# Kernel tuning notes

Measured on AMD Instinct MI355X. Metric: run time of the kernel, lower is better.

Reference implementation:

```python
import jax, jax.numpy as jnp
import numpy as np

B = 256
# (Cin, Cout, K, Hout) for each of the 6 deformable conv layers; input is 33x33
_LAYERS = [(1, 16, 3, 31), (16, 32, 3, 29), (32, 16, 5, 25), (16, 16, 7, 19), (16, 8, 5, 15), (8, 4, 3, 13)]


def setup_inputs() -> dict:
    key = jax.random.key(0)
    ks = jax.random.split(key, 24)
    inp = {"x": jax.random.normal(ks[0], (B, 1, 33, 33), dtype=jnp.float32)}
    for i, (ci, co, k, ho) in enumerate(_LAYERS):
        inp[f"off{i+1}"] = jax.random.normal(ks[1 + i], (1, 2 * k * k, ho, ho), dtype=jnp.float32)
        inp[f"w{i+1}"] = jax.random.normal(ks[7 + i], (co, ci, k, k), dtype=jnp.float32) / float(np.sqrt(ci * k * k))
        inp[f"b{i+1}"] = jnp.zeros((co,), jnp.float32)
    inp["w7"] = jax.random.normal(ks[13], (13 * 13 * 4, 256), dtype=jnp.float32) / 26.0
    inp["b7"] = jnp.zeros((256,), jnp.float32)
    inp["w8"] = jax.random.normal(ks[14], (256, 10), dtype=jnp.float32) / 16.0
    inp["b8"] = jnp.zeros((10,), jnp.float32)
    inp["perm"] = jnp.arange(13 * 13, dtype=jnp.int32)  # fixed spatial permutation (perm_6.ordenar)
    return inp


def _deform_conv(x, offset, weight, bias):
    # torchvision DeformConv2d, stride=1, padding=0, fixed offsets shared across batch.
    Bn, Cin, H, W = x.shape
    Cout, _, K, _ = weight.shape
    Ho, Wo = offset.shape[-2], offset.shape[-1]
    K2 = K * K
    off = offset[0].reshape(K2, 2, Ho, Wo)  # channel layout: [2k]=dy, [2k+1]=dx
    ky, kx = jnp.meshgrid(jnp.arange(K), jnp.arange(K), indexing='ij')
    py = jnp.arange(Ho, dtype=x.dtype)[None, :, None] + ky.reshape(-1, 1, 1) + off[:, 0]  # [K2,Ho,Wo]
    px = jnp.arange(Wo, dtype=x.dtype)[None, None, :] + kx.reshape(-1, 1, 1) + off[:, 1]
    y0f = jnp.floor(py); x0f = jnp.floor(px)
    wy = py - y0f; wx = px - x0f
    y0 = y0f.astype(jnp.int32); x0 = x0f.astype(jnp.int32)
    xf = x.reshape(Bn, Cin, H * W)

    def gather(yi, xi):
        valid = ((yi >= 0) & (yi < H) & (xi >= 0) & (xi < W)).astype(x.dtype)
        idx = (jnp.clip(yi, 0, H - 1) * W + jnp.clip(xi, 0, W - 1)).reshape(-1)
        v = xf[:, :, idx].reshape(Bn, Cin, K2, Ho, Wo)
        return v * valid[None, None]

    s = (gather(y0, x0) * ((1 - wy) * (1 - wx))[None, None]
         + gather(y0, x0 + 1) * ((1 - wy) * wx)[None, None]
         + gather(y0 + 1, x0) * (wy * (1 - wx))[None, None]
         + gather(y0 + 1, x0 + 1) * (wy * wx)[None, None])  # [B,Cin,K2,Ho,Wo]
    out = jnp.einsum('bckhw,ock->bohw', s, weight.reshape(Cout, Cin, K2))
    return out + bias[None, :, None, None]


def reference(x, off1, off2, off3, off4, off5, off6,
              w1, b1, w2, b2, w3, b3, w4, b4, w5, b5, w6, b6,
              w7, b7, w8, b8, perm):
    offs = (off1, off2, off3, off4, off5, off6)
    ws = (w1, w2, w3, w4, w5, w6)
    bs = (b1, b2, b3, b4, b5, b6)
    for off, w, b in zip(offs, ws, bs):
        x = jax.nn.relu(_deform_conv(x, off, w, b))
    Bn = x.shape[0]
    x = x.reshape(Bn, 4, 13 * 13)[:, :, perm].reshape(Bn, -1)  # perm_6.ordenar as spatial permutation
    h = jax.nn.relu(x @ w7 + b7)
    return h @ w8 + b8
```

## Files before the change

kernel.cpp:

```cpp
#include <hip/hip_runtime.h>

template<int N> struct IC { static constexpr int val = N; };

struct WtArgs { const float* src[6]; int co[6], ci[6], k2[6], dstoff[6]; };

__global__ __launch_bounds__(256)
void transpose_weights(WtArgs a, float* __restrict__ dst0)
{
    const int L = blockIdx.x;
    const float* __restrict__ s = a.src[L];
    float* __restrict__ d = dst0 + a.dstoff[L];
    const int co = a.co[L], ci = a.ci[L], k2 = a.k2[L];
    const int n = co * ci * k2;
    for (int i = threadIdx.x; i < n; i += 256) {
        int k = i % k2;
        int c = (i / k2) % ci;
        int o = i / (k2 * ci);
        d[(k * ci + c) * co + o] = s[i];
    }
}

struct MetaArgs { const float* off[6]; int P[6], K[6], WO[6], H[6], W[6], base[6]; };

__global__ __launch_bounds__(256)
void build_meta(MetaArgs a, float* __restrict__ meta0)
{
    const int L = blockIdx.y;
    const float* __restrict__ off = a.off[L];
    const int P = a.P[L], K = a.K[L], WOv = a.WO[L], H = a.H[L], Wv = a.W[L];
    const int N = P * K * K;
    float* __restrict__ m = meta0 + (size_t)a.base[L] * 8;
    for (int e = blockIdx.x * 256 + threadIdx.x; e < N; e += gridDim.x * 256) {
        const int k = e / P, p = e - k * P;
        const int ho = p / WOv, wo = p - ho * WOv;
        const int ky = k / K, kx = k - ky * K;
        const float dy = off[(2 * k)     * P + p];
        const float dx = off[(2 * k + 1) * P + p];
        const float py = (float)(ho + ky) + dy;
        const float px = (float)(wo + kx) + dx;
        const float y0f = floorf(py), x0f = floorf(px);
        const float wy = py - y0f, wx = px - x0f;
        const int y0 = (int)y0f, x0 = (int)x0f;
        const int y1 = y0 + 1,  x1 = x0 + 1;
        const bool vy0 = ((unsigned)y0 < (unsigned)H);
        const bool vy1 = ((unsigned)y1 < (unsigned)H);
        const bool vx0 = ((unsigned)x0 < (unsigned)Wv);
        const bool vx1 = ((unsigned)x1 < (unsigned)Wv);
        const int cy0 = min(max(y0, 0), H - 1) * Wv;
        const int cy1 = min(max(y1, 0), H - 1) * Wv;
        const int cx0 = min(max(x0, 0), Wv - 1);
        const int cx1 = min(max(x1, 0), Wv - 1);
        int4 mi;
        mi.x = cy0 + cx0; mi.y = cy0 + cx1; mi.z = cy1 + cx0; mi.w = cy1 + cx1;
        float4 mw;
        mw.x = (vy0 && vx0) ? (1.f - wy) * (1.f - wx) : 0.f;
        mw.y = (vy0 && vx1) ? (1.f - wy) * wx         : 0.f;
        mw.z = (vy1 && vx0) ? wy * (1.f - wx)         : 0.f;
        mw.w = (vy1 && vx1) ? wy * wx                 : 0.f;
        *(int4*)(m + (size_t)e * 8)       = mi;
        *(float4*)(m + (size_t)e * 8 + 4) = mw;
    }
}

template<int CIN, int CINW, int COUT, int K, int H, int W, int HO, int WO,
         int S, int KSEG, int NT, int NCOMB, bool SPLITOUT, bool MET,
         int NSL = 1, int CINL = 0, int NCHS = 1, int KSPL = 1>
__global__ __launch_bounds__(NT)
void deform_lds(const float* __restrict__ x0, const float* __restrict__ x1,
                const float* __restrict__ x2, const float* __restrict__ x3,
                const float* __restrict__ off, const float* __restrict__ meta,
                const float* __restrict__ wT, const float* __restrict__ bias,
                float* __restrict__ y, size_t pstride)
{
    constexpr int K2 = K * K, HW = H * W, P = HO * WO;
    constexpr int PW = ((P + 63) / 64) * 64;
    constexpr int K2B  = (K2 + KSPL - 1) / KSPL;
    constexpr int KLEN = (K2B + KSEG - 1) / KSEG;
    constexpr int PSTR = (COUT % 2 == 0) ? COUT + 1 : COUT;
    static_assert(NT >= KSEG * PW, "NT too small for KSEG*PW");

    __shared__ __align__(16) float simg[HW * S];
    __shared__ float part[(KSEG > 1) ? (KSEG - 1) * P * PSTR : 1];

    const int tid = threadIdx.x;
    const int b   = blockIdx.x;
    const int hy  = SPLITOUT ? blockIdx.y : 0;
    const int hch = (KSPL > 1) ? (hy % NCHS) : hy;
    const int hk  = (KSPL > 1) ? (hy / NCHS) : 0;

    const size_t xoff = (size_t)b * CINW * HW + (SPLITOUT ? (size_t)hch * CIN * HW : 0);
    const float* xb  = x0 + xoff;
    const float* xb1 = (NCOMB >= 2) ? (x1 + xoff) : nullptr;
    const float* xb2 = (NCOMB >= 3) ? (x2 + xoff) : nullptr;
    const float* xb3 = (NCOMB >= 4) ? (x3 + xoff) : nullptr;
    for (int i = tid; i < CIN * HW; i += NT) {
        int c = i / HW, hw = i - c * HW;
        bool ok = true;
        if constexpr (SPLITOUT) ok = (hch * CIN + c < CINW);
        float v = 0.f;
        if (ok) {
            v = xb[i];
            if constexpr (NCOMB >= 2) v += xb1[i];
            if constexpr (NCOMB >= 3) v += xb2[i];
            if constexpr (NCOMB >= 4) v += xb3[i];
            if constexpr (NCOMB >= 2) v = fmaxf(v, 0.f);
        }
        simg[hw * S + c] = v;
    }
    __syncthreads();

    const int g  = tid / PW;
    const int p  = tid - g * PW;
    const int pc = (p < P) ? p : (P - 1);
    const bool active = (p < P);

    float acc[COUT];
#pragma unroll
    for (int o = 0; o < COUT; ++o) acc[o] = 0.f;

    if (g < KSEG) {
        if ((!SPLITOUT || hy == 0) && g == 0) {
#pragma unroll
            for (int o = 0; o < COUT; ++o) acc[o] = bias[o];
        }
        const int ho = pc / WO, wo = pc - ho * WO;
        const int kb   = hk * K2B + g * KLEN;
        const int kend = (KSPL > 1) ? min(K2, hk * K2B + K2B) : K2;

        auto run = [&](auto nc4tag) {
            constexpr int NC4 = decltype(nc4tag)::val;

            auto fma_block = [&](int i00, int i01, int i10, int i11,
                                 float w00, float w01, float w10, float w11,
                                 int kku) {
                const float* __restrict__ r00 = simg + i00 * S;
                const float* __restrict__ r01 = simg + i01 * S;
                const float* __restrict__ r10 = simg + i10 * S;
                const float* __restrict__ r11 = simg + i11 * S;
                const float* __restrict__ wk = wT + kku * (CINW * COUT)
                                             + (SPLITOUT ? hch * (CIN * COUT) : 0);
                if constexpr (CIN % 4 == 0) {
#pragma unroll
                    for (int c4 = 0; c4 < NC4; ++c4) {
                        const float4 v00 = *(const float4*)(r00 + c4 * 4);
                        const float4 v01 = *(const float4*)(r01 + c4 * 4);
                        const float4 v10 = *(const float4*)(r10 + c4 * 4);
                        const float4 v11 = *(const float4*)(r11 + c4 * 4);
                        float4 sa;
                        sa.x = fmaf(w00, v00.x, fmaf(w01, v01.x, fmaf(w10, v10.x, w11 * v11.x)));
                        sa.y = fmaf(w00, v00.y, fmaf(w01, v01.y, fmaf(w10, v10.y, w11 * v11.y)));
                        sa.z = fmaf(w00, v00.z, fmaf(w01, v01.z, fmaf(w10, v10.z, w11 * v11.z)));
                        sa.w = fmaf(w00, v00.w, fmaf(w01, v01.w, fmaf(w10, v10.w, w11 * v11.w)));
                        const float* __restrict__ wc = wk + (c4 * 4) * COUT;
#pragma unroll
                        for (int o = 0; o < COUT; ++o) acc[o] = fmaf(wc[o], sa.x, acc[o]);
#pragma unroll
                        for (int o = 0; o < COUT; ++o) acc[o] = fmaf(wc[COUT + o], sa.y, acc[o]);
#pragma unroll
                        for (int o = 0; o < COUT; ++o) acc[o] = fmaf(wc[2 * COUT + o], sa.z, acc[o]);
#pragma unroll
                        for (int o = 0; o < COUT; ++o) acc[o] = fmaf(wc[3 * COUT + o], sa.w, acc[o]);
                    }
                } else {
#pragma unroll
                    for (int c = 0; c < CIN; ++c) {
                        float sa = fmaf(w00, r00[c], fmaf(w01, r01[c],
                                   fmaf(w10, r10[c], w11 * r11[c])));
#pragma unroll
                        for (int o = 0; o < COUT; ++o)
                            acc[o] = fmaf(wk[c * COUT + o], sa, acc[o]);
                    }
                }
            };

            if constexpr (MET) {
                const int kf = (kb < K2) ? kb : (K2 - 1);
                int4   nmi = *(const int4*)  (meta + (size_t)(kf * P + pc) * 8);
                float4 nmw = *(const float4*)(meta + (size_t)(kf * P + pc) * 8 + 4);

#pragma unroll 1
                for (int j = 0; j < KLEN; ++j) {
                    const int k  = kb + j;
                    const int kk = (k < K2) ? k : (K2 - 1);
                    const int4   mi  = nmi;
                    const float4 mwv = nmw;
                    const int kn = (k + 1 < K2) ? (k + 1) : (K2 - 1);
                    nmi = *(const int4*)  (meta + (size_t)(kn * P + pc) * 8);
                    nmw = *(const float4*)(meta + (size_t)(kn * P + pc) * 8 + 4);

                    float w00 = mwv.x, w01 = mwv.y, w10 = mwv.z, w11 = mwv.w;
                    if constexpr (K2 % (KSEG * KSPL) != 0) {
                        const float kv = (k < kend) ? 1.f : 0.f;
                        w00 *= kv; w01 *= kv; w10 *= kv; w11 *= kv;
                    }
                    const int kku = __builtin_amdgcn_readfirstlane(kk);
                    fma_block(mi.x, mi.y, mi.z, mi.w, w00, w01, w10, w11, kku);
                }
            } else {
                const int kf = (kb < K2) ? kb : (K2 - 1);
                float ndy = off[(2 * kf)     * P + pc];
                float ndx = off[(2 * kf + 1) * P + pc];

#pragma unroll 1
                for (int j = 0; j < KLEN; ++j) {
                    const int k  = kb + j;
                    const int kk = (k < K2) ? k : (K2 - 1);
                    const float dy = ndy, dx = ndx;
                    const int kn = (k + 1 < K2) ? (k + 1) : (K2 - 1);
                    ndy = off[(2 * kn)     * P + pc];
                    ndx = off[(2 * kn + 1) * P + pc];

                    const int ky = kk / K, kx = kk - ky * K;
                    const float py = (float)(ho + ky) + dy;
                    const float px = (float)(wo + kx) + dx;
                    const float y0f = floorf(py), x0f = floorf(px);
                    const float wy = py - y0f, wx = px - x0f;
                    const int y0 = (int)y0f, x0 = (int)x0f;
                    const int y1 = y0 + 1,  x1i = x0 + 1;
                    const bool vy0 = ((unsigned)y0  < (unsigned)H);
                    const bool vy1 = ((unsigned)y1  < (unsigned)H);
                    const bool vx0 = ((unsigned)x0  < (unsigned)W);
                    const bool vx1 = ((unsigned)x1i < (unsigned)W);
                    const int cy0 = min(max(y0, 0), H - 1) * W;
                    const int cy1 = min(max(y1, 0), H - 1) * W;
                    const int cx0 = min(max(x0, 0), W - 1);
                    const int cx1 = min(max(x1i, 0), W - 1);
                    float w00 = (vy0 && vx0) ? (1.f - wy) * (1.f - wx) : 0.f;
                    float w01 = (vy0 && vx1) ? (1.f - wy) * wx         : 0.f;
                    float w10 = (vy1 && vx0) ? wy * (1.f - wx)         : 0.f;
                    float w11 = (vy1 && vx1) ? wy * wx                 : 0.f;
                    if constexpr (K2 % (KSEG * KSPL) != 0) {
                        const float kv = (k < kend) ? 1.f : 0.f;
                        w00 *= kv; w01 *= kv; w10 *= kv; w11 *= kv;
                    }
                    const int kku = __builtin_amdgcn_readfirstlane(kk);
                    fma_block(cy0 + cx0, cy0 + cx1, cy1 + cx0, cy1 + cx1,
                              w00, w01, w10, w11, kku);
                }
            }
        };

        if constexpr (SPLITOUT && CINL > 0) {
            if (hch == NSL - 1) run(IC<(CINL + 3) / 4>{});
            else                run(IC<(CIN + 3) / 4>{});
        } else {
            run(IC<(CIN + 3) / 4>{});
        }

        if (g > 0 && active) {
#pragma unroll
            for (int o = 0; o < COUT; ++o)
                part[(g - 1) * (P * PSTR) + p * PSTR + o] = acc[o];
        }
    }

    if constexpr (KSEG > 1) __syncthreads();

    if (g == 0 && active) {
        if constexpr (KSEG > 1) {
#pragma unroll
            for (int gg = 1; gg < KSEG; ++gg)
#pragma unroll
                for (int o = 0; o < COUT; ++o)
                    acc[o] += part[(gg - 1) * (P * PSTR) + p * PSTR + o];
        }
        float* yb = y + (SPLITOUT ? (size_t)hy * pstride : 0) + (size_t)b * COUT * P;
#pragma unroll
        for (int o = 0; o < COUT; ++o)
            yb[o * P + p] = SPLITOUT ? acc[o] : fmaxf(acc[o], 0.f);
    }
}

__global__ __launch_bounds__(1024)
void fc_head(const float* __restrict__ x6, const float* __restrict__ w7,
             const float* __restrict__ b7, const float* __restrict__ w8,
             const float* __restrict__ b8, const int* __restrict__ perm,
             float* __restrict__ out)
{
    constexpr int F = 676;
    __shared__ float sx[F];
    __shared__ float ps[3][256];
    __shared__ float sh[256];

    const int tid = threadIdx.x;
    const int b   = blockIdx.x;
    const int j   = tid & 255;
    const int fq  = tid >> 8;

    for (int i = tid; i < F; i += 1024) {
        int c = i / 169, p = i - c * 169;
        sx[i] = x6[(size_t)b * F + c * 169 + perm[p]];
    }
    __syncthreads();

    const int f0 = fq * 169;
    float a = 0.f;
#pragma unroll 4
    for (int i = 0; i < 169; ++i)
        a = fmaf(sx[f0 + i], w7[(size_t)(f0 + i) * 256 + j], a);

    if (fq > 0) ps[fq - 1][j] = a;
    __syncthreads();

    if (fq == 0)
        sh[j] = fmaxf(b7[j] + ((a + ps[0][j]) + (ps[1][j] + ps[2][j])), 0.f);
    __syncthreads();

    if (tid < 10) {
        float acc8 = b8[tid];
#pragma unroll 8
        for (int jj = 0; jj < 256; ++jj)
            acc8 = fmaf(sh[jj], w8[jj * 10 + tid], acc8);
        out[(size_t)b * 10 + tid] = acc8;
    }
}

extern "C" void kernel_launch(void* const* d_in, const int* in_sizes, int n_in,
                              void* d_out, int out_size, void* d_ws, size_t ws_size,
                              hipStream_t stream)
{
    const float* x    = (const float*)d_in[0];
    const float* off1 = (const float*)d_in[1];
    const float* w1   = (const float*)d_in[2];
    const float* b1   = (const float*)d_in[3];
    const float* off2 = (const float*)d_in[4];
    const float* w2   = (const float*)d_in[5];
    const float* b2   = (const float*)d_in[6];
    const float* off3 = (const float*)d_in[7];
    const float* w3   = (const float*)d_in[8];
    const float* b3   = (const float*)d_in[9];
    const float* off4 = (const float*)d_in[10];
    const float* w4   = (const float*)d_in[11];
    const float* b4   = (const float*)d_in[12];
    const float* off5 = (const float*)d_in[13];
    const float* w5   = (const float*)d_in[14];
    const float* b5   = (const float*)d_in[15];
    const float* off6 = (const float*)d_in[16];
    const float* w6   = (const float*)d_in[17];
    const float* b6   = (const float*)d_in[18];
    const float* w7   = (const float*)d_in[19];
    const float* b7   = (const float*)d_in[20];
    const float* w8   = (const float*)d_in[21];
    const float* b8   = (const float*)d_in[22];
    const int*   perm = (const int*)d_in[23];
    float* out = (float*)d_out;

    const int woff[6] = {0, 144, 4752, 17552, 30096, 33296};
    float* ws   = (float*)d_ws;
    float* wt   = ws;
    float* buf0 = ws + 33792;
    float* buf1 = buf0 + 3936256;

    float* a1   = buf0;
    float* a2   = buf1;
    float* p1L2 = ws + 13419520;
    float* a3   = buf0;
    float* p1L3 = ws + 10859520;
    float* a4p0 = buf1;
    float* a5   = buf0;
    float* a6   = buf1;
    float* meta = ws + 20308992;

    const int mbase[6] = {0, 8649, 16218, 31843, 49532, 55157};
    const int MTOT = 56678;

    const bool splitL3 = (ws_size >= (size_t)13419520 * sizeof(float));
    const bool splitL2 = (ws_size >= (size_t)20308992 * sizeof(float));
    const bool metaOK  = (ws_size >= (size_t)(20308992 + MTOT * 8) * sizeof(float));
    const bool split3  = (ws_size >= (size_t)24245248 * sizeof(float));
    const size_t X      = 10825728;
    const size_t pstrL2 = (size_t)(p1L2 - a2);
    const size_t pstrL4 = 1478656;

    WtArgs wa;
    wa.src[0] = w1; wa.src[1] = w2; wa.src[2] = w3;
    wa.src[3] = w4; wa.src[4] = w5; wa.src[5] = w6;
    const int cos[6] = {16, 32, 16, 16, 8, 4};
    const int cis[6] = {1, 16, 32, 16, 16, 8};
    const int k2s[6] = {9, 9, 25, 49, 25, 9};
    for (int i = 0; i < 6; ++i) {
        wa.co[i] = cos[i]; wa.ci[i] = cis[i];
        wa.k2[i] = k2s[i]; wa.dstoff[i] = woff[i];
    }
    transpose_weights<<<dim3(6), dim3(256), 0, stream>>>(wa, wt);

    const dim3 g1(256), g2(256, 2), g3(256, 3);

    if (metaOK) {
        MetaArgs ma;
        ma.off[0] = off1; ma.off[1] = off2; ma.off[2] = off3;
        ma.off[3] = off4; ma.off[4] = off5; ma.off[5] = off6;
        const int Ps[6]  = {961, 841, 625, 361, 225, 169};
        const int Ks[6]  = {3, 3, 5, 7, 5, 3};
        const int WOs[6] = {31, 29, 25, 19, 15, 13};
        const int Hs[6]  = {33, 31, 29, 25, 19, 15};
        const int Ws_[6] = {33, 31, 29, 25, 19, 15};
        for (int i = 0; i < 6; ++i) {
            ma.P[i] = Ps[i]; ma.K[i] = Ks[i]; ma.WO[i] = WOs[i];
            ma.H[i] = Hs[i]; ma.W[i] = Ws_[i]; ma.base[i] = mbase[i];
        }
        build_meta<<<dim3(64, 6), dim3(256), 0, stream>>>(ma, meta);

        deform_lds< 1,  1, 16, 3, 33, 33, 31, 31,  1, 1, 1024, 1, false, true>
            <<<g1, dim3(1024), 0, stream>>>(x, nullptr, nullptr, nullptr, off1, meta + (size_t)mbase[0]*8, wt + woff[0], b1, a1, 0);
        deform_lds< 8, 16, 32, 3, 31, 31, 29, 29, 12, 1,  896, 1, true,  true>
            <<<g2, dim3(896),  0, stream>>>(a1, nullptr, nullptr, nullptr, off2, meta + (size_t)mbase[1]*8, wt + woff[1], b2, a2, pstrL2);

        if (split3) {
            deform_lds<12, 32, 16, 5, 29, 29, 25, 25, 12, 1,  640, 2, true,  true, 3, 8>
                <<<g3, dim3(640),  0, stream>>>(a2, p1L2, nullptr, nullptr, off3, meta + (size_t)mbase[2]*8, wt + woff[2], b3, a3, X);
            deform_lds< 8, 16, 16, 7, 25, 25, 19, 19, 12, 2,  768, 3, true,  true>
                <<<g2, dim3(768),  0, stream>>>(a3, a3 + X, a3 + 2 * X, nullptr, off4, meta + (size_t)mbase[3]*8, wt + woff[3], b4, a4p0, pstrL4);
        } else {
            deform_lds<16, 32, 16, 5, 29, 29, 25, 25, 20, 1,  640, 2, true,  true>
                <<<g2, dim3(640),  0, stream>>>(a2, p1L2, nullptr, nullptr, off3, meta + (size_t)mbase[2]*8, wt + woff[2], b3, a3, X);
            deform_lds< 8, 16, 16, 7, 25, 25, 19, 19, 12, 2,  768, 2, true,  true>
                <<<g2, dim3(768),  0, stream>>>(a3, a3 + X, nullptr, nullptr, off4, meta + (size_t)mbase[3]*8, wt + woff[3], b4, a4p0, pstrL4);
        }

        deform_lds<16, 16,  8, 5, 19, 19, 15, 15, 20, 4, 1024, 2, false, true>
            <<<g1, dim3(1024), 0, stream>>>(a4p0, a4p0 + pstrL4, nullptr, nullptr, off5, meta + (size_t)mbase[4]*8, wt + woff[4], b5, a5, 0);
        deform_lds< 8,  8,  4, 3, 15, 15, 13, 13, 12, 5,  960, 1, false, true>
            <<<g1, dim3(960),  0, stream>>>(a5, nullptr, nullptr, nullptr, off6, meta + (size_t)mbase[5]*8, wt + woff[5], b6, a6, 0);
    } else {
        deform_lds< 1,  1, 16, 3, 33, 33, 31, 31,  1, 1, 1024, 1, false, false>
            <<<g1, dim3(1024), 0, stream>>>(x, nullptr, nullptr, nullptr, off1, nullptr, wt + woff[0], b1, a1, 0);
        if (splitL2) {
            deform_lds< 8, 16, 32, 3, 31, 31, 29, 29, 12, 1, 1024, 1, true, false>
                <<<g2, dim3(1024), 0, stream>>>(a1, nullptr, nullptr, nullptr, off2, nullptr, wt + woff[1], b2, a2, pstrL2);
        } else {
            deform_lds<16, 16, 32, 3, 31, 31, 29, 29, 20, 1, 1024, 1, false, false>
                <<<g1, dim3(1024), 0, stream>>>(a1, nullptr, nullptr, nullptr, off2, nullptr, wt + woff[1], b2, a2, 0);
        }
        if (splitL3) {
            if (splitL2) {
                deform_lds<16, 32, 16, 5, 29, 29, 25, 25, 20, 1, 1024, 2, true, false>
                    <<<g2, dim3(1024), 0, stream>>>(a2, p1L2, nullptr, nullptr, off3, nullptr, wt + woff[2], b3, a3, X);
            } else {
                deform_lds<16, 32, 16, 5, 29, 29, 25, 25, 20, 1, 1024, 1, true, false>
                    <<<g2, dim3(1024), 0, stream>>>(a2, nullptr, nullptr, nullptr, off3, nullptr, wt + woff[2], b3, a3, X);
            }
            deform_lds< 8, 16, 16, 7, 25, 25, 19, 19, 12, 2,  768, 2, true, false>
                <<<g2, dim3(768),  0, stream>>>(a3, a3 + X, nullptr, nullptr, off4, nullptr, wt + woff[3], b4, a4p0, pstrL4);
        } else {
            deform_lds<32, 32, 16, 5, 29, 29, 25, 25, 36, 1, 1024, 1, false, false>
                <<<g1, dim3(1024), 0, stream>>>(a2, nullptr, nullptr, nullptr, off3, nullptr, wt + woff[2], b3, a3, 0);
            deform_lds< 8, 16, 16, 7, 25, 25, 19, 19, 12, 2,  768, 1, true, false>
                <<<g2, dim3(768),  0, stream>>>(a3, nullptr, nullptr, nullptr, off4, nullptr, wt + woff[3], b4, a4p0, pstrL4);
        }
        deform_lds<16, 16,  8, 5, 19, 19, 15, 15, 20, 4, 1024, 2, false, false>
            <<<g1, dim3(1024), 0, stream>>>(a4p0, a4p0 + pstrL4, nullptr, nullptr, off5, nullptr, wt + woff[4], b5, a5, 0);
        deform_lds< 8,  8,  4, 3, 15, 15, 13, 13, 12, 5,  960, 1, false, false>
            <<<g1, dim3(960),  0, stream>>>(a5, nullptr, nullptr, nullptr, off6, nullptr, wt + woff[5], b6, a6, 0);
    }

    fc_head<<<dim3(256), dim3(1024), 0, stream>>>(a6, w7, b7, w8, b8, perm, out);
}
```

Baseline: 237.5 us.

## Fuse deformable layers 5, 6 and FC head into one per-sample kernel

Replaces the last two deformable conv launches and the FC head with a single kernel per batch sample. Layer-5 input is staged in LDS, and layer-5 and layer-6 activations stay in shared memory, with per-group k-split partial sums reduced through LDS. The FC layers then run in the same block. This removes two kernel launches and the global round trips for a5 and a6. In exchange it uses a large LDS footprint per block, which lowers occupancy, and fixes the thread mapping for layers 5 and 6.

```diff
diff --git a/kernel.cpp b/kernel.cpp
--- a/kernel.cpp
+++ b/kernel.cpp
@@ -272,6 +272,225 @@
 }
 
 __global__ __launch_bounds__(1024)
+void tail_fused(const float* __restrict__ a4p0, const float* __restrict__ a4p1,
+                const float* __restrict__ meta5, const float* __restrict__ meta6,
+                const float* __restrict__ wt5, const float* __restrict__ b5,
+                const float* __restrict__ wt6, const float* __restrict__ b6,
+                const float* __restrict__ w7, const float* __restrict__ b7,
+                const float* __restrict__ w8, const float* __restrict__ b8,
+                const int* __restrict__ perm, float* __restrict__ out)
+{
+    constexpr int HW5 = 361, P5 = 225, K25 = 25, S5 = 20;
+    constexpr int HW6 = 225, P6 = 169, K26 = 9,  S6 = 12;
+
+    __shared__ __align__(16) float simg5[HW5 * S5];
+    __shared__ float part5[3 * P5 * 9];
+    __shared__ __align__(16) float act5[HW6 * S6];
+    __shared__ float part6[4 * P6 * 5];
+    __shared__ float a6l[676];
+    __shared__ float sx[676];
+    __shared__ float ps[3][256];
+    __shared__ float sh[256];
+
+    const int tid = threadIdx.x;
+    const int b   = blockIdx.x;
+
+    {
+        const size_t boff = (size_t)b * 16 * HW5;
+        for (int i = tid; i < 16 * HW5; i += 1024) {
+            int c = i / HW5, hw = i - c * HW5;
+            simg5[hw * S5 + c] = fmaxf(a4p0[boff + i] + a4p1[boff + i], 0.f);
+        }
+    }
+    __syncthreads();
+
+    {
+        const int g  = tid >> 8;
+        const int p  = tid & 255;
+        const int pc = (p < P5) ? p : (P5 - 1);
+        const bool active = (p < P5);
+
+        float acc[8];
+#pragma unroll
+        for (int o = 0; o < 8; ++o) acc[o] = (g == 0) ? b5[o] : 0.f;
+
+        const int kb = g * 7;
+        const int kf = (kb < K25) ? kb : (K25 - 1);
+        int4   nmi = *(const int4*)  (meta5 + (size_t)(kf * P5 + pc) * 8);
+        float4 nmw = *(const float4*)(meta5 + (size_t)(kf * P5 + pc) * 8 + 4);
+
+#pragma unroll 1
+        for (int j = 0; j < 7; ++j) {
+            const int k  = kb + j;
+            const int kk = (k < K25) ? k : (K25 - 1);
+            const int4   mi  = nmi;
+            const float4 mwv = nmw;
+            const int kn = (k + 1 < K25) ? (k + 1) : (K25 - 1);
+            nmi = *(const int4*)  (meta5 + (size_t)(kn * P5 + pc) * 8);
+            nmw = *(const float4*)(meta5 + (size_t)(kn * P5 + pc) * 8 + 4);
+
+            const float kv = (k < K25) ? 1.f : 0.f;
+            const float w00 = mwv.x * kv, w01 = mwv.y * kv;
+            const float w10 = mwv.z * kv, w11 = mwv.w * kv;
+            const int kku = __builtin_amdgcn_readfirstlane(kk);
+            const float* __restrict__ wk = wt5 + kku * 128;
+            const float* __restrict__ r00 = simg5 + mi.x * S5;
+            const float* __restrict__ r01 = simg5 + mi.y * S5;
+            const float* __restrict__ r10 = simg5 + mi.z * S5;
+            const float* __restrict__ r11 = simg5 + mi.w * S5;
+#pragma unroll
+            for (int c4 = 0; c4 < 4; ++c4) {
+                const float4 v00 = *(const float4*)(r00 + c4 * 4);
+                const float4 v01 = *(const float4*)(r01 + c4 * 4);
+                const float4 v10 = *(const float4*)(r10 + c4 * 4);
+                const float4 v11 = *(const float4*)(r11 + c4 * 4);
+                float4 sa;
+                sa.x = fmaf(w00, v00.x, fmaf(w01, v01.x, fmaf(w10, v10.x, w11 * v11.x)));
+                sa.y = fmaf(w00, v00.y, fmaf(w01, v01.y, fmaf(w10, v10.y, w11 * v11.y)));
+                sa.z = fmaf(w00, v00.z, fmaf(w01, v01.z, fmaf(w10, v10.z, w11 * v11.z)));
+                sa.w = fmaf(w00, v00.w, fmaf(w01, v01.w, fmaf(w10, v10.w, w11 * v11.w)));
+                const float* __restrict__ wc = wk + c4 * 32;
+#pragma unroll
+                for (int o = 0; o < 8; ++o) acc[o] = fmaf(wc[o],      sa.x, acc[o]);
+#pragma unroll
+                for (int o = 0; o < 8; ++o) acc[o] = fmaf(wc[8 + o],  sa.y, acc[o]);
+#pragma unroll
+                for (int o = 0; o < 8; ++o) acc[o] = fmaf(wc[16 + o], sa.z, acc[o]);
+#pragma unroll
+                for (int o = 0; o < 8; ++o) acc[o] = fmaf(wc[24 + o], sa.w, acc[o]);
+            }
+        }
+
+        if (g > 0 && active) {
+#pragma unroll
+            for (int o = 0; o < 8; ++o)
+                part5[(g - 1) * (P5 * 9) + p * 9 + o] = acc[o];
+        }
+        __syncthreads();
+
+        if (g == 0 && active) {
+#pragma unroll
+            for (int gg = 1; gg < 4; ++gg)
+#pragma unroll
+                for (int o = 0; o < 8; ++o)
+                    acc[o] += part5[(gg - 1) * (P5 * 9) + p * 9 + o];
+#pragma unroll
+            for (int o = 0; o < 8; ++o)
+                act5[p * S6 + o] = fmaxf(acc[o], 0.f);
+        }
+    }
+    __syncthreads();
+
+    {
+        const int g  = tid / 192;
+        const int p  = tid - g * 192;
+        const int pc = (p < P6) ? p : (P6 - 1);
+        const bool active = (p < P6) && (g < 5);
+
+        float acc[4];
+#pragma unroll
+        for (int o = 0; o < 4; ++o) acc[o] = (g == 0) ? b6[o] : 0.f;
+
+        if (g < 5) {
+            const int kb = g * 2;
+            const int kf = (kb < K26) ? kb : (K26 - 1);
+            int4   nmi = *(const int4*)  (meta6 + (size_t)(kf * P6 + pc) * 8);
+            float4 nmw = *(const float4*)(meta6 + (size_t)(kf * P6 + pc) * 8 + 4);
+
+#pragma unroll 1
+            for (int j = 0; j < 2; ++j) {
+                const int k  = kb + j;
+                const int kk = (k < K26) ? k : (K26 - 1);
+                const int4   mi  = nmi;
+                const float4 mwv = nmw;
+                const int kn = (k + 1 < K26) ? (k + 1) : (K26 - 1);
+                nmi = *(const int4*)  (meta6 + (size_t)(kn * P6 + pc) * 8);
+                nmw = *(const float4*)(meta6 + (size_t)(kn * P6 + pc) * 8 + 4);
+
+                const float kv = (k < K26) ? 1.f : 0.f;
+                const float w00 = mwv.x * kv, w01 = mwv.y * kv;
+                const float w10 = mwv.z * kv, w11 = mwv.w * kv;
+                const int kku = __builtin_amdgcn_readfirstlane(kk);
+                const float* __restrict__ wk = wt6 + kku * 32;
+                const float* __restrict__ r00 = act5 + mi.x * S6;
+                const float* __restrict__ r01 = act5 + mi.y * S6;
+                const float* __restrict__ r10 = act5 + mi.z * S6;
+                const float* __restrict__ r11 = act5 + mi.w * S6;
+#pragma unroll
+                for (int c4 = 0; c4 < 2; ++c4) {
+                    const float4 v00 = *(const float4*)(r00 + c4 * 4);
+                    const float4 v01 = *(const float4*)(r01 + c4 * 4);
+                    const float4 v10 = *(const float4*)(r10 + c4 * 4);
+                    const float4 v11 = *(const float4*)(r11 + c4 * 4);
+                    float4 sa;
+                    sa.x = fmaf(w00, v00.x, fmaf(w01, v01.x, fmaf(w10, v10.x, w11 * v11.x)));
+                    sa.y = fmaf(w00, v00.y, fmaf(w01, v01.y, fmaf(w10, v10.y, w11 * v11.y)));
+                    sa.z = fmaf(w00, v00.z, fmaf(w01, v01.z, fmaf(w10, v10.z, w11 * v11.z)));
+                    sa.w = fmaf(w00, v00.w, fmaf(w01, v01.w, fmaf(w10, v10.w, w11 * v11.w)));
+                    const float* __restrict__ wc = wk + c4 * 16;
+#pragma unroll
+                    for (int o = 0; o < 4; ++o) acc[o] = fmaf(wc[o],      sa.x, acc[o]);
+#pragma unroll
+                    for (int o = 0; o < 4; ++o) acc[o] = fmaf(wc[4 + o],  sa.y, acc[o]);
+#pragma unroll
+                    for (int o = 0; o < 4; ++o) acc[o] = fmaf(wc[8 + o],  sa.z, acc[o]);
+#pragma unroll
+                    for (int o = 0; o < 4; ++o) acc[o] = fmaf(wc[12 + o], sa.w, acc[o]);
+                }
+            }
+
+            if (g > 0 && active) {
+#pragma unroll
+                for (int o = 0; o < 4; ++o)
+                    part6[(g - 1) * (P6 * 5) + p * 5 + o] = acc[o];
+            }
+        }
+        __syncthreads();
+
+        if (g == 0 && active) {
+#pragma unroll
+            for (int gg = 1; gg < 5; ++gg)
+#pragma unroll
+                for (int o = 0; o < 4; ++o)
+                    acc[o] += part6[(gg - 1) * (P6 * 5) + p * 5 + o];
+#pragma unroll
+            for (int o = 0; o < 4; ++o)
+                a6l[o * P6 + p] = fmaxf(acc[o], 0.f);
+        }
+    }
+    __syncthreads();
+
+    if (tid < 676) {
+        const int c = tid / 169, pp = tid - c * 169;
+        sx[tid] = a6l[c * 169 + perm[pp]];
+    }
+    __syncthreads();
+
+    {
+        const int j  = tid & 255;
+        const int fq = tid >> 8;
+        const int f0 = fq * 169;
+        float a = 0.f;
+#pragma unroll 4
+        for (int i = 0; i < 169; ++i)
+            a = fmaf(sx[f0 + i], w7[(size_t)(f0 + i) * 256 + j], a);
+        if (fq > 0) ps[fq - 1][j] = a;
+        __syncthreads();
+        if (fq == 0)
+            sh[j] = fmaxf(b7[j] + ((a + ps[0][j]) + (ps[1][j] + ps[2][j])), 0.f);
+    }
+    __syncthreads();
+
+    if (tid < 10) {
+        float acc8 = b8[tid];
+#pragma unroll 8
+        for (int jj = 0; jj < 256; ++jj)
+            acc8 = fmaf(sh[jj], w8[jj * 10 + tid], acc8);
+        out[(size_t)b * 10 + tid] = acc8;
+    }
+}
+
+__global__ __launch_bounds__(1024)
 void fc_head(const float* __restrict__ x6, const float* __restrict__ w7,
              const float* __restrict__ b7, const float* __restrict__ w8,
              const float* __restrict__ b8, const int* __restrict__ perm,
@@ -418,10 +637,11 @@
                 <<<g2, dim3(768),  0, stream>>>(a3, a3 + X, nullptr, nullptr, off4, meta + (size_t)mbase[3]*8, wt + woff[3], b4, a4p0, pstrL4);
         }
 
-        deform_lds<16, 16,  8, 5, 19, 19, 15, 15, 20, 4, 1024, 2, false, true>
-            <<<g1, dim3(1024), 0, stream>>>(a4p0, a4p0 + pstrL4, nullptr, nullptr, off5, meta + (size_t)mbase[4]*8, wt + woff[4], b5, a5, 0);
-        deform_lds< 8,  8,  4, 3, 15, 15, 13, 13, 12, 5,  960, 1, false, true>
-            <<<g1, dim3(960),  0, stream>>>(a5, nullptr, nullptr, nullptr, off6, meta + (size_t)mbase[5]*8, wt + woff[5], b6, a6, 0);
+        tail_fused<<<g1, dim3(1024), 0, stream>>>(
+            a4p0, a4p0 + pstrL4,
+            meta + (size_t)mbase[4]*8, meta + (size_t)mbase[5]*8,
+            wt + woff[4], b5, wt + woff[5], b6,
+            w7, b7, w8, b8, perm, out);
     } else {
         deform_lds< 1,  1, 16, 3, 33, 33, 31, 31,  1, 1, 1024, 1, false, false>
             <<<g1, dim3(1024), 0, stream>>>(x, nullptr, nullptr, nullptr, off1, nullptr, wt + woff[0], b1, a1, 0);
@@ -452,7 +672,6 @@
             <<<g1, dim3(1024), 0, stream>>>(a4p0, a4p0 + pstrL4, nullptr, nullptr, off5, nullptr, wt + woff[4], b5, a5, 0);
         deform_lds< 8,  8,  4, 3, 15, 15, 13, 13, 12, 5,  960, 1, false, false>
             <<<g1, dim3(960),  0, stream>>>(a5, nullptr, nullptr, nullptr, off6, nullptr, wt + woff[5], b6, a6, 0);
-    }
-
-    fc_head<<<dim3(256), dim3(1024), 0, stream>>>(a6, w7, b7, w8, b8, perm, out);
+        fc_head<<<dim3(256), dim3(1024), 0, stream>>>(a6, w7, b7, w8, b8, perm, out);
+    }
 }
```

Measured after the change: 233.2 us. Within noise of the previous version (-1.8%).
